# Performance work log

Hardware: AMD Instinct MI355X
Metric: run time of the kernel (lower is better)

Reference implementation:

```python
import jax, jax.numpy as jnp
import numpy as np

N_NODES = 100_000
N_EDGES = 1_000_000
D_IN = 64
D_OUT = 64
N_TYPES = 16  # get_options().in_dim; must exceed gate types 9/11 referenced in source


def setup_inputs() -> dict:
    key = jax.random.key(0)
    k = jax.random.split(key, 6)
    feat = jax.random.normal(k[0], (N_NODES, D_IN), dtype=jnp.float32)
    src = jax.random.randint(k[1], (N_EDGES,), 0, N_NODES, dtype=jnp.int32)
    dst = jax.random.randint(k[2], (N_EDGES,), 0, N_NODES, dtype=jnp.int32)
    ntype2 = jax.random.randint(k[3], (N_NODES,), 0, N_TYPES, dtype=jnp.int32)
    # per-type Linear params; xavier-uniform-ish (gain=sqrt(2) for relu)
    limit = np.sqrt(2.0) * np.sqrt(6.0 / (D_IN + D_OUT))
    gate_W = jax.random.uniform(k[4], (N_TYPES, D_IN, D_OUT), jnp.float32, -limit, limit)
    gate_b = jax.random.uniform(k[5], (N_TYPES, D_OUT), jnp.float32, -0.1, 0.1)
    return {"feat": feat, "gate_W": gate_W, "gate_b": gate_b,
            "src": src, "dst": dst, "ntype2": ntype2, "act_flag": 1}


def reference(feat, gate_W, gate_b, src, dst, ntype2, act_flag):
    n = feat.shape[0]
    # update_all(copy_src('h','m'), mean('m','neigh')): gather + segment-mean
    msg = feat[src]                                                  # [E, D_in]
    summed = jax.ops.segment_sum(msg, dst, num_segments=n)           # [N, D_in]
    deg = jax.ops.segment_sum(jnp.ones_like(dst, dtype=feat.dtype), dst, num_segments=n)
    neigh = summed / jnp.maximum(deg, 1.0)[:, None]                  # zero-degree -> 0 (DGL default)
    # apply_nodes_func: route each node through Linear_t with t = ntype2[node]
    # compute all T small GEMMs, then select per node (T is small and fixed)
    out_all = jnp.einsum('nd,tdo->nto', neigh, gate_W) + gate_b[None, :, :]   # [N, T, D_out]
    rst = jnp.take_along_axis(out_all, ntype2.astype(jnp.int32)[:, None, None], axis=1)[:, 0, :]
    # activation is None in this configuration, so act_flag is a no-op
    return rst
```

## Files before the change

### kernel.cpp

```cpp
#include <hip/hip_runtime.h>
#include <hip/hip_bf16.h>

#define N_NODES 100000
#define N_EDGES 1000000
#define D 64
#define N_TYPES 16

#define NPB 128
#define NBUCK ((N_NODES + NPB - 1) / NPB)
#define NBLK 256
#define CHUNK ((N_EDGES + NBLK - 1) / NBLK)
#define NB 391
#define ECAP 2560
#define NCHUNK_MAX (N_TYPES + (N_NODES + 63) / 64)

#define WS_TBL    0
#define WS_BTOT   (WS_TBL + NBUCK * NBLK)
#define WS_BSTART (WS_BTOT + NBUCK)
#define WS_TTBL   (WS_BSTART + NBUCK + 1)
#define WS_TOFF   (WS_TTBL + N_TYPES * NB)
#define WS_NLIST  (WS_TOFF + N_TYPES + 1)
#define WS_EBUF   (WS_NLIST + N_NODES)
#define WS_TOTAL  (WS_EBUF + N_EDGES + 64)

__global__ void __launch_bounds__(256)
hist_all(const int* __restrict__ dst, const int* __restrict__ ntype2,
         int* __restrict__ tbl, int* __restrict__ ttbl) {
    __shared__ int hb[NBUCK];
    __shared__ int ht[N_TYPES];
    int b = blockIdx.x, tid = threadIdx.x;
    for (int i = tid; i < NBUCK; i += 256) hb[i] = 0;
    if (tid < N_TYPES) ht[tid] = 0;
    __syncthreads();
    if (b < NBLK) {
        int beg = b * CHUNK, end = min(beg + CHUNK, N_EDGES);
        for (int e = beg + tid; e < end; e += 256)
            atomicAdd(&hb[dst[e] >> 7], 1);
    }
    int n = b * 256 + tid;
    if (n < N_NODES) atomicAdd(&ht[ntype2[n]], 1);
    __syncthreads();
    if (b < NBLK)
        for (int i = tid; i < NBUCK; i += 256) tbl[i * NBLK + b] = hb[i];
    if (tid < N_TYPES) ttbl[tid * NB + b] = ht[tid];
}

__global__ void __launch_bounds__(512)
scan_cols(int* __restrict__ tbl, int* __restrict__ btot) {
    int wave = blockIdx.x * 8 + (threadIdx.x >> 6);
    int lane = threadIdx.x & 63;
    if (wave >= NBUCK) return;
    int4 v = ((int4*)(tbl + wave * NBLK))[lane];
    int s01 = v.x + v.y;
    int s = s01 + v.z + v.w;
    int incl = s;
    for (int o = 1; o < 64; o <<= 1) {
        int u = __shfl_up(incl, o, 64);
        if (lane >= o) incl += u;
    }
    int excl = incl - s;
    int4 w;
    w.x = excl; w.y = excl + v.x; w.z = excl + s01; w.w = excl + s01 + v.z;
    ((int4*)(tbl + wave * NBLK))[lane] = w;
    if (lane == 63) btot[wave] = incl;
}

__global__ void __launch_bounds__(1024)
scan_small(const int* __restrict__ btot, int* __restrict__ bstart,
           int* __restrict__ ttbl, int* __restrict__ toff) {
    __shared__ int sh[1024];
    __shared__ int stot[N_TYPES];
    int t = threadIdx.x;
    int v = (t < NBUCK) ? btot[t] : 0;
    sh[t] = v;
    __syncthreads();
    for (int o = 1; o < 1024; o <<= 1) {
        int u = (t >= o) ? sh[t - o] : 0;
        __syncthreads();
        sh[t] += u;
        __syncthreads();
    }
    if (t <= NBUCK) bstart[t] = sh[t] - v;
    int w = t >> 6, lane = t & 63, base = w * NB;
    int vals[7];
    int s = 0;
#pragma unroll
    for (int j = 0; j < 7; ++j) {
        int idx = lane * 7 + j;
        vals[j] = (idx < NB) ? ttbl[base + idx] : 0;
        s += vals[j];
    }
    int incl = s;
    for (int o = 1; o < 64; o <<= 1) {
        int u = __shfl_up(incl, o, 64);
        if (lane >= o) incl += u;
    }
    int run = incl - s;
#pragma unroll
    for (int j = 0; j < 7; ++j) {
        int idx = lane * 7 + j;
        if (idx < NB) ttbl[base + idx] = run;
        run += vals[j];
    }
    if (lane == 63) stot[w] = incl;
    __syncthreads();
    if (t == 0) {
        int r = 0;
        for (int k = 0; k < N_TYPES; ++k) { toff[k] = r; r += stot[k]; }
        toff[N_TYPES] = r;
    }
}

__global__ void __launch_bounds__(512)
place_all(const int* __restrict__ src, const int* __restrict__ dst,
          const int* __restrict__ ntype2,
          const int* __restrict__ tbl, const int* __restrict__ bstart,
          const int* __restrict__ ttbl, const int* __restrict__ toff,
          unsigned* __restrict__ ebuf, int* __restrict__ nlist) {
    __shared__ int cur[NBUCK];
    __shared__ int tcur[N_TYPES];
    int b = blockIdx.x, tid = threadIdx.x;
    if (b < NBLK)
        for (int i = tid; i < NBUCK; i += 512)
            cur[i] = bstart[i] + tbl[i * NBLK + b];
    if (tid < N_TYPES) tcur[tid] = toff[tid] + ttbl[tid * NB + b];
    __syncthreads();
    if (b < NBLK) {
        int beg = b * CHUNK, end = min(beg + CHUNK, N_EDGES);
        for (int e = beg + tid; e < end; e += 512) {
            int d = dst[e];
            int slot = atomicAdd(&cur[d >> 7], 1);
            ebuf[slot] = ((unsigned)(d & (NPB - 1)) << 20) | (unsigned)src[e];
        }
    }
    if (tid < 256) {
        int n = b * 256 + tid;
        if (n < N_NODES) {
            int ty = ntype2[n];
            int p = atomicAdd(&tcur[ty], 1);
            nlist[p] = n;
        }
    }
}

__global__ void __launch_bounds__(512)
bucket_gather(const float* __restrict__ feat,
              const int* __restrict__ bstart, const unsigned* __restrict__ ebuf,
              float* __restrict__ out) {
    __shared__ int hist[NPB];
    __shared__ int offL[NPB];
    __shared__ int curL[NPB];
    __shared__ int sortedL[ECAP];

    int k = blockIdx.x, tid = threadIdx.x;
    for (int i = tid; i < NPB; i += 512) hist[i] = 0;
    __syncthreads();
    int beg = bstart[k];
    int ecnt = bstart[k + 1] - beg;
    if (ecnt > ECAP) ecnt = ECAP;
    for (int i = tid; i < ecnt; i += 512)
        atomicAdd(&hist[ebuf[beg + i] >> 20], 1);
    __syncthreads();
    if (tid == 0) {
        int r = 0;
        for (int n = 0; n < NPB; ++n) { offL[n] = r; curL[n] = r; r += hist[n]; }
    }
    __syncthreads();
    for (int i = tid; i < ecnt; i += 512) {
        unsigned p = ebuf[beg + i];
        int pos = atomicAdd(&curL[p >> 20], 1);
        sortedL[pos] = (int)(p & 0xFFFFFu);
    }
    __syncthreads();

    int wv = tid >> 6, lane = tid & 63;
    int sub = lane >> 5, h = lane & 31;
    const float2* __restrict__ F = (const float2*)feat;
    int node0 = k * NPB;
#pragma unroll
    for (int it = 0; it < 8; ++it) {
        int n = (wv * 8 + it) * 2 + sub;
        int cnt = hist[n], o = offL[n];
        float sx = 0.0f, sy = 0.0f;
        int j = 0;
        for (; j + 4 <= cnt; j += 4) {
            int s0 = sortedL[o + j + 0];
            int s1 = sortedL[o + j + 1];
            int s2 = sortedL[o + j + 2];
            int s3 = sortedL[o + j + 3];
            float2 v0 = F[s0 * 32 + h];
            float2 v1 = F[s1 * 32 + h];
            float2 v2 = F[s2 * 32 + h];
            float2 v3 = F[s3 * 32 + h];
            sx += (v0.x + v1.x) + (v2.x + v3.x);
            sy += (v0.y + v1.y) + (v2.y + v3.y);
        }
        for (; j < cnt; ++j) {
            int s = sortedL[o + j];
            float2 v = F[s * 32 + h];
            sx += v.x; sy += v.y;
        }
        float scale = (cnt > 1) ? (1.0f / (float)cnt) : 1.0f;
        int node = node0 + n;
        if (node < N_NODES) {
            float2 r; r.x = sx * scale; r.y = sy * scale;
            ((float2*)out)[node * 32 + h] = r;
        }
    }
}

__global__ void __launch_bounds__(256)
apply_typed(const float* __restrict__ gate_W, const float* __restrict__ gate_b,
            const int* __restrict__ toff, const int* __restrict__ nlist,
            float* __restrict__ out) {
    __shared__ float rowbuf[4][D];
    int b = blockIdx.x;
    int t = 0, c0 = 0, acc = 0; bool found = false;
#pragma unroll
    for (int k = 0; k < N_TYPES; ++k) {
        int cnt = toff[k + 1] - toff[k];
        int nch = (cnt + 63) >> 6;
        if (!found && b < acc + nch) { t = k; c0 = b - acc; found = true; }
        acc += nch;
    }
    if (!found) return;

    int lane = threadIdx.x & 63;
    int wv = threadIdx.x >> 6;
    const float* __restrict__ W = gate_W + t * D * D;
    float wreg[D];
#pragma unroll
    for (int d = 0; d < D; ++d) wreg[d] = W[d * D + lane];
    float bias = gate_b[t * D + lane];

    int beg = toff[t] + c0 * 64;
    int lim = toff[t + 1] - beg; if (lim > 64) lim = 64;

    for (int i = wv; i < lim; i += 4) {
        int node = nlist[beg + i];
        float nv = out[node * D + lane];
        rowbuf[wv][lane] = nv;
        float a0 = bias, a1 = 0.0f, a2 = 0.0f, a3 = 0.0f;
#pragma unroll
        for (int d = 0; d < D; d += 4) {
            float4 av = *(const float4*)&rowbuf[wv][d];
            a0 = fmaf(av.x, wreg[d + 0], a0);
            a1 = fmaf(av.y, wreg[d + 1], a1);
            a2 = fmaf(av.z, wreg[d + 2], a2);
            a3 = fmaf(av.w, wreg[d + 3], a3);
        }
        out[node * D + lane] = (a0 + a1) + (a2 + a3);
    }
}

__global__ void scatter_feat(const float* __restrict__ feat, const int* __restrict__ src,
                             const int* __restrict__ dst, float* __restrict__ accum) {
    long long idx = (long long)blockIdx.x * blockDim.x + threadIdx.x;
    if (idx >= (long long)N_EDGES * D) return;
    int e = (int)(idx >> 6), d = (int)(idx & 63);
    atomicAdd(accum + dst[e] * D + d, feat[src[e] * D + d]);
}
__global__ void scatter_deg(const int* __restrict__ dst, float* __restrict__ deg) {
    int e = blockIdx.x * blockDim.x + threadIdx.x;
    if (e >= N_EDGES) return;
    atomicAdd(deg + dst[e], 1.0f);
}
__global__ void apply_linear(const float* __restrict__ gate_W, const float* __restrict__ gate_b,
                             const int* __restrict__ ntype2, const float* __restrict__ deg,
                             float* __restrict__ out) {
    int node = blockIdx.x * (blockDim.x >> 6) + (threadIdx.x >> 6);
    int lane = threadIdx.x & 63;
    if (node >= N_NODES) return;
    int t = ntype2[node];
    float dv = deg[node]; dv = dv > 1.0f ? dv : 1.0f;
    float nv = out[node * D + lane] / dv;
    const float* W = gate_W + t * D * D;
    float acc = gate_b[t * D + lane];
#pragma unroll 16
    for (int d = 0; d < D; ++d)
        acc = fmaf(__shfl(nv, d, 64), W[d * D + lane], acc);
    out[node * D + lane] = acc;
}

extern "C" void kernel_launch(void* const* d_in, const int* in_sizes, int n_in,
                              void* d_out, int out_size, void* d_ws, size_t ws_size,
                              hipStream_t stream) {
    const float* feat   = (const float*)d_in[0];
    const float* gate_W = (const float*)d_in[1];
    const float* gate_b = (const float*)d_in[2];
    const int*   src    = (const int*)d_in[3];
    const int*   dst    = (const int*)d_in[4];
    const int*   ntype2 = (const int*)d_in[5];
    float* out = (float*)d_out;

    if (ws_size >= (size_t)WS_TOTAL * 4) {
        int* ws = (int*)d_ws;
        int* tbl       = ws + WS_TBL;
        int* btot      = ws + WS_BTOT;
        int* bstart    = ws + WS_BSTART;
        int* ttbl      = ws + WS_TTBL;
        int* toff      = ws + WS_TOFF;
        int* nlist     = ws + WS_NLIST;
        unsigned* ebuf = (unsigned*)(ws + WS_EBUF);

        hist_all<<<NB, 256, 0, stream>>>(dst, ntype2, tbl, ttbl);
        scan_cols<<<(NBUCK + 7) / 8, 512, 0, stream>>>(tbl, btot);
        scan_small<<<1, 1024, 0, stream>>>(btot, bstart, ttbl, toff);
        place_all<<<NB, 512, 0, stream>>>(src, dst, ntype2, tbl, bstart,
                                          ttbl, toff, ebuf, nlist);
        bucket_gather<<<NBUCK, 512, 0, stream>>>(feat, bstart, ebuf, out);
        apply_typed<<<NCHUNK_MAX, 256, 0, stream>>>(gate_W, gate_b, toff, nlist, out);
    } else {
        float* deg = (float*)d_ws;
        hipMemsetAsync(out, 0, sizeof(float) * N_NODES * D, stream);
        hipMemsetAsync(deg, 0, sizeof(float) * N_NODES, stream);
        long long total = (long long)N_EDGES * D;
        scatter_feat<<<(int)((total + 255) / 256), 256, 0, stream>>>(feat, src, dst, out);
        scatter_deg<<<(N_EDGES + 255) / 256, 256, 0, stream>>>(dst, deg);
        apply_linear<<<(N_NODES + 3) / 4, 256, 0, stream>>>(gate_W, gate_b, ntype2, deg, out);
    }
}
```

Measured before the change: 190.1 us.

## Fuse typed linear into bucket gather and stage edge placement in shared memory

The per-type GEMM now runs inside the bucket-gather kernel. Each block keeps its 128 aggregated rows in shared memory, sorts its nodes by type, and reloads weights only when the type changes, so the separate type histogram, scan, node list and apply kernel are gone. The out buffer is no longer written and then read back. Edge placement first sorts each chunk locally in shared memory by bucket and then writes to ebuf in a coalesced pass. The cost is much larger shared-memory use per block (a 32 KB row buffer plus staging), which may limit occupancy, and ECAP drops to 2048, which risks truncating high-degree buckets.

```diff
diff --git a/kernel.cpp b/kernel.cpp
--- a/kernel.cpp
+++ b/kernel.cpp
@@ -1,5 +1,4 @@
 #include <hip/hip_runtime.h>
-#include <hip/hip_bf16.h>
 
 #define N_NODES 100000
 #define N_EDGES 1000000
@@ -10,39 +9,25 @@
 #define NBUCK ((N_NODES + NPB - 1) / NPB)
 #define NBLK 256
 #define CHUNK ((N_EDGES + NBLK - 1) / NBLK)
-#define NB 391
-#define ECAP 2560
-#define NCHUNK_MAX (N_TYPES + (N_NODES + 63) / 64)
+#define ECAP 2048
 
 #define WS_TBL    0
 #define WS_BTOT   (WS_TBL + NBUCK * NBLK)
 #define WS_BSTART (WS_BTOT + NBUCK)
-#define WS_TTBL   (WS_BSTART + NBUCK + 1)
-#define WS_TOFF   (WS_TTBL + N_TYPES * NB)
-#define WS_NLIST  (WS_TOFF + N_TYPES + 1)
-#define WS_EBUF   (WS_NLIST + N_NODES)
+#define WS_EBUF   (WS_BSTART + NBUCK + 1)
 #define WS_TOTAL  (WS_EBUF + N_EDGES + 64)
 
 __global__ void __launch_bounds__(256)
-hist_all(const int* __restrict__ dst, const int* __restrict__ ntype2,
-         int* __restrict__ tbl, int* __restrict__ ttbl) {
+hist_edges(const int* __restrict__ dst, int* __restrict__ tbl) {
     __shared__ int hb[NBUCK];
-    __shared__ int ht[N_TYPES];
     int b = blockIdx.x, tid = threadIdx.x;
     for (int i = tid; i < NBUCK; i += 256) hb[i] = 0;
-    if (tid < N_TYPES) ht[tid] = 0;
-    __syncthreads();
-    if (b < NBLK) {
-        int beg = b * CHUNK, end = min(beg + CHUNK, N_EDGES);
-        for (int e = beg + tid; e < end; e += 256)
-            atomicAdd(&hb[dst[e] >> 7], 1);
-    }
-    int n = b * 256 + tid;
-    if (n < N_NODES) atomicAdd(&ht[ntype2[n]], 1);
-    __syncthreads();
-    if (b < NBLK)
-        for (int i = tid; i < NBUCK; i += 256) tbl[i * NBLK + b] = hb[i];
-    if (tid < N_TYPES) ttbl[tid * NB + b] = ht[tid];
+    __syncthreads();
+    int beg = b * CHUNK, end = min(beg + CHUNK, N_EDGES);
+    for (int e = beg + tid; e < end; e += 256)
+        atomicAdd(&hb[dst[e] >> 7], 1);
+    __syncthreads();
+    for (int i = tid; i < NBUCK; i += 256) tbl[i * NBLK + b] = hb[i];
 }
 
 __global__ void __launch_bounds__(512)
@@ -66,10 +51,8 @@
 }
 
 __global__ void __launch_bounds__(1024)
-scan_small(const int* __restrict__ btot, int* __restrict__ bstart,
-           int* __restrict__ ttbl, int* __restrict__ toff) {
+scan_buckets(const int* __restrict__ btot, int* __restrict__ bstart) {
     __shared__ int sh[1024];
-    __shared__ int stot[N_TYPES];
     int t = threadIdx.x;
     int v = (t < NBUCK) ? btot[t] : 0;
     sh[t] = v;
@@ -81,78 +64,86 @@
         __syncthreads();
     }
     if (t <= NBUCK) bstart[t] = sh[t] - v;
-    int w = t >> 6, lane = t & 63, base = w * NB;
-    int vals[7];
-    int s = 0;
-#pragma unroll
-    for (int j = 0; j < 7; ++j) {
-        int idx = lane * 7 + j;
-        vals[j] = (idx < NB) ? ttbl[base + idx] : 0;
-        s += vals[j];
-    }
+}
+
+__global__ void __launch_bounds__(512)
+place_staged(const int* __restrict__ src, const int* __restrict__ dst,
+             const int* __restrict__ tbl, const int* __restrict__ bstart,
+             unsigned* __restrict__ ebuf) {
+    __shared__ int hb[NBUCK];
+    __shared__ int lo[NBUCK];
+    __shared__ int gb[NBUCK];
+    __shared__ int cur[NBUCK];
+    __shared__ uint2 stage[CHUNK];
+    __shared__ int wpart[8];
+
+    int b = blockIdx.x, tid = threadIdx.x;
+    int lane = tid & 63, wv = tid >> 6;
+    for (int i = tid; i < NBUCK; i += 512) hb[i] = 0;
+    __syncthreads();
+    int beg = b * CHUNK, end = min(beg + CHUNK, N_EDGES);
+    for (int e = beg + tid; e < end; e += 512)
+        atomicAdd(&hb[dst[e] >> 7], 1);
+    __syncthreads();
+
+    int i0 = 2 * tid, i1 = 2 * tid + 1;
+    int a0 = (i0 < NBUCK) ? hb[i0] : 0;
+    int a1 = (i1 < NBUCK) ? hb[i1] : 0;
+    int s = a0 + a1;
     int incl = s;
     for (int o = 1; o < 64; o <<= 1) {
         int u = __shfl_up(incl, o, 64);
         if (lane >= o) incl += u;
     }
-    int run = incl - s;
-#pragma unroll
-    for (int j = 0; j < 7; ++j) {
-        int idx = lane * 7 + j;
-        if (idx < NB) ttbl[base + idx] = run;
-        run += vals[j];
-    }
-    if (lane == 63) stot[w] = incl;
-    __syncthreads();
-    if (t == 0) {
+    if (lane == 63) wpart[wv] = incl;
+    __syncthreads();
+    if (tid == 0) {
         int r = 0;
-        for (int k = 0; k < N_TYPES; ++k) { toff[k] = r; r += stot[k]; }
-        toff[N_TYPES] = r;
-    }
-}
-
-__global__ void __launch_bounds__(512)
-place_all(const int* __restrict__ src, const int* __restrict__ dst,
-          const int* __restrict__ ntype2,
-          const int* __restrict__ tbl, const int* __restrict__ bstart,
-          const int* __restrict__ ttbl, const int* __restrict__ toff,
-          unsigned* __restrict__ ebuf, int* __restrict__ nlist) {
-    __shared__ int cur[NBUCK];
-    __shared__ int tcur[N_TYPES];
-    int b = blockIdx.x, tid = threadIdx.x;
-    if (b < NBLK)
-        for (int i = tid; i < NBUCK; i += 512)
-            cur[i] = bstart[i] + tbl[i * NBLK + b];
-    if (tid < N_TYPES) tcur[tid] = toff[tid] + ttbl[tid * NB + b];
-    __syncthreads();
-    if (b < NBLK) {
-        int beg = b * CHUNK, end = min(beg + CHUNK, N_EDGES);
-        for (int e = beg + tid; e < end; e += 512) {
-            int d = dst[e];
-            int slot = atomicAdd(&cur[d >> 7], 1);
-            ebuf[slot] = ((unsigned)(d & (NPB - 1)) << 20) | (unsigned)src[e];
-        }
-    }
-    if (tid < 256) {
-        int n = b * 256 + tid;
-        if (n < N_NODES) {
-            int ty = ntype2[n];
-            int p = atomicAdd(&tcur[ty], 1);
-            nlist[p] = n;
-        }
-    }
-}
-
-__global__ void __launch_bounds__(512)
-bucket_gather(const float* __restrict__ feat,
-              const int* __restrict__ bstart, const unsigned* __restrict__ ebuf,
-              float* __restrict__ out) {
+        for (int w = 0; w < 8; ++w) { int tmp = wpart[w]; wpart[w] = r; r += tmp; }
+    }
+    __syncthreads();
+    incl += wpart[wv];
+    int excl = incl - s;
+    if (i0 < NBUCK) lo[i0] = excl;
+    if (i1 < NBUCK) lo[i1] = excl + a0;
+    __syncthreads();
+    for (int i = tid; i < NBUCK; i += 512) {
+        gb[i] = bstart[i] + tbl[i * NBLK + b] - lo[i];
+        cur[i] = lo[i];
+    }
+    __syncthreads();
+    for (int e = beg + tid; e < end; e += 512) {
+        int d = dst[e];
+        int pos = atomicAdd(&cur[d >> 7], 1);
+        uint2 v; v.x = (unsigned)d; v.y = (unsigned)src[e];
+        stage[pos] = v;
+    }
+    __syncthreads();
+    int cnt = end - beg;
+    for (int idx = tid; idx < cnt; idx += 512) {
+        uint2 v = stage[idx];
+        int bk = (int)(v.x >> 7);
+        ebuf[gb[bk] + idx] = ((v.x & (NPB - 1)) << 20) | v.y;
+    }
+}
+
+__global__ void __launch_bounds__(512, 2)
+bucket_conv(const float* __restrict__ feat,
+            const float* __restrict__ gate_W, const float* __restrict__ gate_b,
+            const int* __restrict__ ntype2,
+            const int* __restrict__ bstart, const unsigned* __restrict__ ebuf,
+            float* __restrict__ out) {
     __shared__ int hist[NPB];
     __shared__ int offL[NPB];
     __shared__ int curL[NPB];
     __shared__ int sortedL[ECAP];
+    __shared__ float rowfull[NPB * D];
+    __shared__ unsigned char ord[NPB];
+    __shared__ unsigned char typ[NPB];
+    __shared__ int tc[N_TYPES], tb[N_TYPES], tcur[N_TYPES];
 
     int k = blockIdx.x, tid = threadIdx.x;
+    int lane = tid & 63, wv = tid >> 6;
     for (int i = tid; i < NPB; i += 512) hist[i] = 0;
     __syncthreads();
     int beg = bstart[k];
@@ -173,7 +164,6 @@
     }
     __syncthreads();
 
-    int wv = tid >> 6, lane = tid & 63;
     int sub = lane >> 5, h = lane & 31;
     const float2* __restrict__ F = (const float2*)feat;
     int node0 = k * NPB;
@@ -201,55 +191,53 @@
             sx += v.x; sy += v.y;
         }
         float scale = (cnt > 1) ? (1.0f / (float)cnt) : 1.0f;
-        int node = node0 + n;
-        if (node < N_NODES) {
-            float2 r; r.x = sx * scale; r.y = sy * scale;
-            ((float2*)out)[node * 32 + h] = r;
+        float2 r; r.x = sx * scale; r.y = sy * scale;
+        ((float2*)rowfull)[n * 32 + h] = r;
+    }
+
+    int nvalid = N_NODES - node0; if (nvalid > NPB) nvalid = NPB;
+    if (tid < N_TYPES) tc[tid] = 0;
+    __syncthreads();
+    int myt = -1;
+    if (tid < nvalid) { myt = ntype2[node0 + tid]; atomicAdd(&tc[myt], 1); }
+    __syncthreads();
+    if (tid == 0) {
+        int r = 0;
+        for (int t = 0; t < N_TYPES; ++t) { tb[t] = r; tcur[t] = r; r += tc[t]; }
+    }
+    __syncthreads();
+    if (tid < nvalid) {
+        int p = atomicAdd(&tcur[myt], 1);
+        ord[p] = (unsigned char)tid;
+        typ[p] = (unsigned char)myt;
+    }
+    __syncthreads();
+
+    int i0 = wv * 16, i1 = i0 + 16; if (i1 > nvalid) i1 = nvalid;
+    int tprev = -1;
+    float wreg[D];
+    float bias = 0.0f;
+    for (int i = i0; i < i1; ++i) {
+        int n = (int)ord[i];
+        int t = (int)typ[i];
+        if (t != tprev) {
+            tprev = t;
+            const float* __restrict__ W = gate_W + t * D * D;
+#pragma unroll
+            for (int d = 0; d < D; ++d) wreg[d] = W[d * D + lane];
+            bias = gate_b[t * D + lane];
         }
-    }
-}
-
-__global__ void __launch_bounds__(256)
-apply_typed(const float* __restrict__ gate_W, const float* __restrict__ gate_b,
-            const int* __restrict__ toff, const int* __restrict__ nlist,
-            float* __restrict__ out) {
-    __shared__ float rowbuf[4][D];
-    int b = blockIdx.x;
-    int t = 0, c0 = 0, acc = 0; bool found = false;
-#pragma unroll
-    for (int k = 0; k < N_TYPES; ++k) {
-        int cnt = toff[k + 1] - toff[k];
-        int nch = (cnt + 63) >> 6;
-        if (!found && b < acc + nch) { t = k; c0 = b - acc; found = true; }
-        acc += nch;
-    }
-    if (!found) return;
-
-    int lane = threadIdx.x & 63;
-    int wv = threadIdx.x >> 6;
-    const float* __restrict__ W = gate_W + t * D * D;
-    float wreg[D];
-#pragma unroll
-    for (int d = 0; d < D; ++d) wreg[d] = W[d * D + lane];
-    float bias = gate_b[t * D + lane];
-
-    int beg = toff[t] + c0 * 64;
-    int lim = toff[t + 1] - beg; if (lim > 64) lim = 64;
-
-    for (int i = wv; i < lim; i += 4) {
-        int node = nlist[beg + i];
-        float nv = out[node * D + lane];
-        rowbuf[wv][lane] = nv;
+        const float* __restrict__ ar = &rowfull[n * D];
         float a0 = bias, a1 = 0.0f, a2 = 0.0f, a3 = 0.0f;
 #pragma unroll
         for (int d = 0; d < D; d += 4) {
-            float4 av = *(const float4*)&rowbuf[wv][d];
+            float4 av = *(const float4*)(ar + d);
             a0 = fmaf(av.x, wreg[d + 0], a0);
             a1 = fmaf(av.y, wreg[d + 1], a1);
             a2 = fmaf(av.z, wreg[d + 2], a2);
             a3 = fmaf(av.w, wreg[d + 3], a3);
         }
-        out[node * D + lane] = (a0 + a1) + (a2 + a3);
+        out[(node0 + n) * D + lane] = (a0 + a1) + (a2 + a3);
     }
 }
 
@@ -298,18 +286,14 @@
         int* tbl       = ws + WS_TBL;
         int* btot      = ws + WS_BTOT;
         int* bstart    = ws + WS_BSTART;
-        int* ttbl      = ws + WS_TTBL;
-        int* toff      = ws + WS_TOFF;
-        int* nlist     = ws + WS_NLIST;
         unsigned* ebuf = (unsigned*)(ws + WS_EBUF);
 
-        hist_all<<<NB, 256, 0, stream>>>(dst, ntype2, tbl, ttbl);
+        hist_edges<<<NBLK, 256, 0, stream>>>(dst, tbl);
         scan_cols<<<(NBUCK + 7) / 8, 512, 0, stream>>>(tbl, btot);
-        scan_small<<<1, 1024, 0, stream>>>(btot, bstart, ttbl, toff);
-        place_all<<<NB, 512, 0, stream>>>(src, dst, ntype2, tbl, bstart,
-                                          ttbl, toff, ebuf, nlist);
-        bucket_gather<<<NBUCK, 512, 0, stream>>>(feat, bstart, ebuf, out);
-        apply_typed<<<NCHUNK_MAX, 256, 0, stream>>>(gate_W, gate_b, toff, nlist, out);
+        scan_buckets<<<1, 1024, 0, stream>>>(btot, bstart);
+        place_staged<<<NBLK, 512, 0, stream>>>(src, dst, tbl, bstart, ebuf);
+        bucket_conv<<<NBUCK, 512, 0, stream>>>(feat, gate_W, gate_b, ntype2,
+                                               bstart, ebuf, out);
     } else {
         float* deg = (float*)d_ws;
         hipMemsetAsync(out, 0, sizeof(float) * N_NODES * D, stream);
```

After: 180.7 us. 1.05x faster.

## Fuse histogram, scans and placement into one cooperative kernel with grid syncs

Applied to the files above, without the earlier changes.

Replaces four separate sort-prep kernels (histogram, column scan, small scan, placement) with a single cooperative kernel that uses grid.sync between phases, keeping each block's edges in registers across phases. Placement now stages edges in shared memory sorted by bucket so that writes to the global edge buffer are contiguous per bucket, instead of scattered per edge. This is meant to remove launch overhead and the repeated global reloads of dst/src. In exchange it relies on all 256 blocks being co-resident, uses a large shared staging buffer, and ECAP is lowered to 2048.

```diff
diff --git a/kernel.cpp b/kernel.cpp
--- a/kernel.cpp
+++ b/kernel.cpp
@@ -1,5 +1,7 @@
 #include <hip/hip_runtime.h>
-#include <hip/hip_bf16.h>
+#include <hip/hip_cooperative_groups.h>
+
+namespace cg = cooperative_groups;
 
 #define N_NODES 100000
 #define N_EDGES 1000000
@@ -10,136 +12,179 @@
 #define NBUCK ((N_NODES + NPB - 1) / NPB)
 #define NBLK 256
 #define CHUNK ((N_EDGES + NBLK - 1) / NBLK)
-#define NB 391
-#define ECAP 2560
+#define EPT 8
+#define NODES_PB ((N_NODES + NBLK - 1) / NBLK)
+#define ECAP 2048
 #define NCHUNK_MAX (N_TYPES + (N_NODES + 63) / 64)
 
 #define WS_TBL    0
 #define WS_BTOT   (WS_TBL + NBUCK * NBLK)
 #define WS_BSTART (WS_BTOT + NBUCK)
 #define WS_TTBL   (WS_BSTART + NBUCK + 1)
-#define WS_TOFF   (WS_TTBL + N_TYPES * NB)
+#define WS_TOFF   (WS_TTBL + N_TYPES * NBLK)
 #define WS_NLIST  (WS_TOFF + N_TYPES + 1)
 #define WS_EBUF   (WS_NLIST + N_NODES)
 #define WS_TOTAL  (WS_EBUF + N_EDGES + 64)
 
-__global__ void __launch_bounds__(256)
-hist_all(const int* __restrict__ dst, const int* __restrict__ ntype2,
-         int* __restrict__ tbl, int* __restrict__ ttbl) {
+__global__ void __launch_bounds__(512)
+coop_sort(const int* __restrict__ src, const int* __restrict__ dst,
+          const int* __restrict__ ntype2,
+          int* __restrict__ tbl, int* __restrict__ btot, int* __restrict__ bstart,
+          int* __restrict__ ttbl, int* __restrict__ toff,
+          int* __restrict__ nlist, unsigned* __restrict__ ebuf) {
+    cg::grid_group grid = cg::this_grid();
     __shared__ int hb[NBUCK];
+    __shared__ int gb[NBUCK];
+    __shared__ uint2 stage[CHUNK];
+    __shared__ int wpart[8];
     __shared__ int ht[N_TYPES];
+    __shared__ int stot[N_TYPES];
+
     int b = blockIdx.x, tid = threadIdx.x;
-    for (int i = tid; i < NBUCK; i += 256) hb[i] = 0;
+    int lane = tid & 63, wv = tid >> 6;
+
+    int beg = b * CHUNK, end = min(beg + CHUNK, N_EDGES);
+    int ed[EPT], es[EPT];
+#pragma unroll
+    for (int j = 0; j < EPT; ++j) {
+        int e = beg + tid + j * 512;
+        ed[j] = (e < end) ? dst[e] : -1;
+        es[j] = (e < end) ? src[e] : 0;
+    }
+    for (int i = tid; i < NBUCK; i += 512) hb[i] = 0;
     if (tid < N_TYPES) ht[tid] = 0;
     __syncthreads();
-    if (b < NBLK) {
-        int beg = b * CHUNK, end = min(beg + CHUNK, N_EDGES);
-        for (int e = beg + tid; e < end; e += 256)
-            atomicAdd(&hb[dst[e] >> 7], 1);
-    }
-    int n = b * 256 + tid;
-    if (n < N_NODES) atomicAdd(&ht[ntype2[n]], 1);
-    __syncthreads();
-    if (b < NBLK)
-        for (int i = tid; i < NBUCK; i += 256) tbl[i * NBLK + b] = hb[i];
-    if (tid < N_TYPES) ttbl[tid * NB + b] = ht[tid];
-}
-
-__global__ void __launch_bounds__(512)
-scan_cols(int* __restrict__ tbl, int* __restrict__ btot) {
-    int wave = blockIdx.x * 8 + (threadIdx.x >> 6);
-    int lane = threadIdx.x & 63;
-    if (wave >= NBUCK) return;
-    int4 v = ((int4*)(tbl + wave * NBLK))[lane];
-    int s01 = v.x + v.y;
-    int s = s01 + v.z + v.w;
+#pragma unroll
+    for (int j = 0; j < EPT; ++j)
+        if (ed[j] >= 0) atomicAdd(&hb[ed[j] >> 7], 1);
+    int mynode = b * NODES_PB + tid;
+    int myt = -1;
+    if (tid < NODES_PB && mynode < N_NODES) {
+        myt = ntype2[mynode];
+        atomicAdd(&ht[myt], 1);
+    }
+    __syncthreads();
+    for (int i = tid; i < NBUCK; i += 512) tbl[i * NBLK + b] = hb[i];
+    if (tid < N_TYPES) ttbl[tid * NBLK + b] = ht[tid];
+
+    grid.sync();
+
+    int gw = b * 8 + wv;
+    if (gw < NBUCK) {
+        int4 v = ((int4*)(tbl + gw * NBLK))[lane];
+        int s01 = v.x + v.y;
+        int s = s01 + v.z + v.w;
+        int incl = s;
+        for (int o = 1; o < 64; o <<= 1) {
+            int u = __shfl_up(incl, o, 64);
+            if (lane >= o) incl += u;
+        }
+        int excl = incl - s;
+        int4 w;
+        w.x = excl; w.y = excl + v.x; w.z = excl + s01; w.w = excl + s01 + v.z;
+        ((int4*)(tbl + gw * NBLK))[lane] = w;
+        if (lane == 63) btot[gw] = incl;
+    }
+
+    grid.sync();
+
+    if (b == 0) {
+        int i0 = 2 * tid, i1 = i0 + 1;
+        int v0 = (i0 < NBUCK) ? btot[i0] : 0;
+        int v1 = (i1 < NBUCK) ? btot[i1] : 0;
+        int s = v0 + v1;
+        int incl = s;
+        for (int o = 1; o < 64; o <<= 1) {
+            int u = __shfl_up(incl, o, 64);
+            if (lane >= o) incl += u;
+        }
+        if (lane == 63) wpart[wv] = incl;
+        __syncthreads();
+        if (tid == 0) {
+            int r = 0;
+            for (int w = 0; w < 8; ++w) { int t2 = wpart[w]; wpart[w] = r; r += t2; }
+        }
+        __syncthreads();
+        int excl = incl - s + wpart[wv];
+        if (i0 <= NBUCK) bstart[i0] = excl;
+        if (i1 <= NBUCK) bstart[i1] = excl + v0;
+    } else if (b == 1) {
+        for (int t = wv; t < N_TYPES; t += 8) {
+            int4 v = ((int4*)(ttbl + t * NBLK))[lane];
+            int s01 = v.x + v.y;
+            int s = s01 + v.z + v.w;
+            int incl = s;
+            for (int o = 1; o < 64; o <<= 1) {
+                int u = __shfl_up(incl, o, 64);
+                if (lane >= o) incl += u;
+            }
+            int excl = incl - s;
+            int4 w;
+            w.x = excl; w.y = excl + v.x; w.z = excl + s01; w.w = excl + s01 + v.z;
+            ((int4*)(ttbl + t * NBLK))[lane] = w;
+            if (lane == 63) stot[t] = incl;
+        }
+        __syncthreads();
+        if (tid == 0) {
+            int r = 0;
+            for (int t = 0; t < N_TYPES; ++t) { toff[t] = r; r += stot[t]; }
+            toff[N_TYPES] = r;
+        }
+    }
+
+    grid.sync();
+
+    for (int i = tid; i < NBUCK; i += 512) hb[i] = 0;
+    __syncthreads();
+#pragma unroll
+    for (int j = 0; j < EPT; ++j)
+        if (ed[j] >= 0) atomicAdd(&hb[ed[j] >> 7], 1);
+    __syncthreads();
+    int i0 = 2 * tid, i1 = i0 + 1;
+    int a0 = (i0 < NBUCK) ? hb[i0] : 0;
+    int a1 = (i1 < NBUCK) ? hb[i1] : 0;
+    int s = a0 + a1;
     int incl = s;
     for (int o = 1; o < 64; o <<= 1) {
         int u = __shfl_up(incl, o, 64);
         if (lane >= o) incl += u;
     }
-    int excl = incl - s;
-    int4 w;
-    w.x = excl; w.y = excl + v.x; w.z = excl + s01; w.w = excl + s01 + v.z;
-    ((int4*)(tbl + wave * NBLK))[lane] = w;
-    if (lane == 63) btot[wave] = incl;
-}
-
-__global__ void __launch_bounds__(1024)
-scan_small(const int* __restrict__ btot, int* __restrict__ bstart,
-           int* __restrict__ ttbl, int* __restrict__ toff) {
-    __shared__ int sh[1024];
-    __shared__ int stot[N_TYPES];
-    int t = threadIdx.x;
-    int v = (t < NBUCK) ? btot[t] : 0;
-    sh[t] = v;
-    __syncthreads();
-    for (int o = 1; o < 1024; o <<= 1) {
-        int u = (t >= o) ? sh[t - o] : 0;
-        __syncthreads();
-        sh[t] += u;
-        __syncthreads();
-    }
-    if (t <= NBUCK) bstart[t] = sh[t] - v;
-    int w = t >> 6, lane = t & 63, base = w * NB;
-    int vals[7];
-    int s = 0;
-#pragma unroll
-    for (int j = 0; j < 7; ++j) {
-        int idx = lane * 7 + j;
-        vals[j] = (idx < NB) ? ttbl[base + idx] : 0;
-        s += vals[j];
-    }
-    int incl = s;
-    for (int o = 1; o < 64; o <<= 1) {
-        int u = __shfl_up(incl, o, 64);
-        if (lane >= o) incl += u;
-    }
-    int run = incl - s;
-#pragma unroll
-    for (int j = 0; j < 7; ++j) {
-        int idx = lane * 7 + j;
-        if (idx < NB) ttbl[base + idx] = run;
-        run += vals[j];
-    }
-    if (lane == 63) stot[w] = incl;
-    __syncthreads();
-    if (t == 0) {
+    if (lane == 63) wpart[wv] = incl;
+    __syncthreads();
+    if (tid == 0) {
         int r = 0;
-        for (int k = 0; k < N_TYPES; ++k) { toff[k] = r; r += stot[k]; }
-        toff[N_TYPES] = r;
-    }
-}
-
-__global__ void __launch_bounds__(512)
-place_all(const int* __restrict__ src, const int* __restrict__ dst,
-          const int* __restrict__ ntype2,
-          const int* __restrict__ tbl, const int* __restrict__ bstart,
-          const int* __restrict__ ttbl, const int* __restrict__ toff,
-          unsigned* __restrict__ ebuf, int* __restrict__ nlist) {
-    __shared__ int cur[NBUCK];
-    __shared__ int tcur[N_TYPES];
-    int b = blockIdx.x, tid = threadIdx.x;
-    if (b < NBLK)
-        for (int i = tid; i < NBUCK; i += 512)
-            cur[i] = bstart[i] + tbl[i * NBLK + b];
-    if (tid < N_TYPES) tcur[tid] = toff[tid] + ttbl[tid * NB + b];
-    __syncthreads();
-    if (b < NBLK) {
-        int beg = b * CHUNK, end = min(beg + CHUNK, N_EDGES);
-        for (int e = beg + tid; e < end; e += 512) {
-            int d = dst[e];
-            int slot = atomicAdd(&cur[d >> 7], 1);
-            ebuf[slot] = ((unsigned)(d & (NPB - 1)) << 20) | (unsigned)src[e];
-        }
-    }
-    if (tid < 256) {
-        int n = b * 256 + tid;
-        if (n < N_NODES) {
-            int ty = ntype2[n];
-            int p = atomicAdd(&tcur[ty], 1);
-            nlist[p] = n;
-        }
+        for (int w = 0; w < 8; ++w) { int t2 = wpart[w]; wpart[w] = r; r += t2; }
+    }
+    __syncthreads();
+    int run = incl - s + wpart[wv];
+    if (i0 < NBUCK) {
+        gb[i0] = bstart[i0] + tbl[i0 * NBLK + b] - run;
+        hb[i0] = run;
+    }
+    if (i1 < NBUCK) {
+        gb[i1] = bstart[i1] + tbl[i1 * NBLK + b] - (run + a0);
+        hb[i1] = run + a0;
+    }
+    __syncthreads();
+#pragma unroll
+    for (int j = 0; j < EPT; ++j) {
+        if (ed[j] >= 0) {
+            int pos = atomicAdd(&hb[ed[j] >> 7], 1);
+            uint2 v; v.x = (unsigned)ed[j]; v.y = (unsigned)es[j];
+            stage[pos] = v;
+        }
+    }
+    if (tid < N_TYPES) ht[tid] = toff[tid] + ttbl[tid * NBLK + b];
+    __syncthreads();
+    int cnt = end - beg;
+    for (int idx = tid; idx < cnt; idx += 512) {
+        uint2 v = stage[idx];
+        int bk = (int)(v.x >> 7);
+        ebuf[gb[bk] + idx] = ((v.x & (NPB - 1)) << 20) | v.y;
+    }
+    if (myt >= 0) {
+        int p = atomicAdd(&ht[myt], 1);
+        nlist[p] = mynode;
     }
 }
 
@@ -303,11 +348,11 @@
         int* nlist     = ws + WS_NLIST;
         unsigned* ebuf = (unsigned*)(ws + WS_EBUF);
 
-        hist_all<<<NB, 256, 0, stream>>>(dst, ntype2, tbl, ttbl);
-        scan_cols<<<(NBUCK + 7) / 8, 512, 0, stream>>>(tbl, btot);
-        scan_small<<<1, 1024, 0, stream>>>(btot, bstart, ttbl, toff);
-        place_all<<<NB, 512, 0, stream>>>(src, dst, ntype2, tbl, bstart,
-                                          ttbl, toff, ebuf, nlist);
+        void* args[] = {(void*)&src, (void*)&dst, (void*)&ntype2,
+                        (void*)&tbl, (void*)&btot, (void*)&bstart,
+                        (void*)&ttbl, (void*)&toff, (void*)&nlist, (void*)&ebuf};
+        hipLaunchCooperativeKernel((void*)coop_sort, dim3(NBLK), dim3(512),
+                                   args, 0, stream);
         bucket_gather<<<NBUCK, 512, 0, stream>>>(feat, bstart, ebuf, out);
         apply_typed<<<NCHUNK_MAX, 256, 0, stream>>>(gate_W, gate_b, toff, nlist, out);
     } else {
```

Measured after the change: 283.5 us. 1.49x slower.
